# Kernel tuning notes

Hardware: AMD Instinct MI355X
Metric: run time of the kernel (lower is better)

The kernel has to match this reference:

```python
import jax, jax.numpy as jnp
import numpy as np

C = 64
G = 4          # group_number
K = 3          # kernel_size
R = 4          # reduction_ratio -> bottleneck C//R = 16
BN_EPS = 1e-3  # keras BatchNormalization default epsilon


def setup_inputs() -> dict:
    key = jax.random.key(0)
    ks = jax.random.split(key, 8)
    B, H, W = 8, 192, 192
    cr = C // R
    x = jax.random.normal(ks[0], (B, H, W, C), dtype=jnp.float32)
    # kernel_gen: Conv2D 1x1 (C -> C//R), BN, ReLU, Conv2D 1x1 (C//R -> K*K*G)
    w1 = jax.random.normal(ks[1], (C, cr), dtype=jnp.float32) * (1.0 / np.sqrt(C))
    b1 = jnp.zeros((cr,), dtype=jnp.float32)
    gamma = 1.0 + 0.1 * jax.random.normal(ks[2], (cr,), dtype=jnp.float32)
    beta = 0.1 * jax.random.normal(ks[3], (cr,), dtype=jnp.float32)
    mean = 0.1 * jax.random.normal(ks[4], (cr,), dtype=jnp.float32)
    var = jax.random.uniform(ks[5], (cr,), dtype=jnp.float32, minval=0.5, maxval=1.5)
    w2 = jax.random.normal(ks[6], (cr, K * K * G), dtype=jnp.float32) * (1.0 / np.sqrt(cr))
    b2 = jnp.zeros((K * K * G,), dtype=jnp.float32)
    return {"x": x, "w1": w1, "b1": b1, "gamma": gamma, "beta": beta,
            "mean": mean, "var": var, "w2": w2, "b2": b2}


def reference(x, w1, b1, gamma, beta, mean, var, w2, b2):
    B, H, W, Cc = x.shape
    # --- kernel generation (stride=1 -> identity pooling) ---
    t = jnp.einsum('bhwc,cd->bhwd', x, w1) + b1                 # [B,H,W,C//R]
    t = (t - mean) * jax.lax.rsqrt(var + BN_EPS) * gamma + beta  # BN (inference)
    t = jax.nn.relu(t)
    kern = jnp.einsum('bhwd,de->bhwe', t, w2) + b2               # [B,H,W,K*K*G]
    kern = kern.reshape(B, H, W, K * K, 1, G)
    # --- unfold: tf.image.extract_patches SAME, stride 1, patch order (ki,kj,C) ---
    pad = K // 2
    xp = jnp.pad(x, ((0, 0), (pad, pad), (pad, pad), (0, 0)))
    patches = jnp.stack(
        [xp[:, i:i + H, j:j + W, :] for i in range(K) for j in range(K)],
        axis=3)                                                  # [B,H,W,K*K,C]
    unfolded = patches.reshape(B, H, W, K * K, Cc // G, G)
    # --- per-pixel multiply-reduce over patch axis ---
    out = jnp.sum(kern * unfolded, axis=3)                       # [B,H,W,C//G,G]
    return out.reshape(B, H, W, Cc)
```

## Files before the change

kernel.cpp:

```cpp
#include <hip/hip_runtime.h>


#define B_   8
#define H_   192
#define W_   192
#define CR_  16
#define TH_  8
#define TW_  16
#define TILES_X (W_/TW_)
#define TILES_PER_IMG (TILES_X*(H_/TH_))
#define NBLK (B_*TILES_PER_IMG)
#define NPIX (TH_*TW_)

constexpr float BN_EPS = 1e-3f;

template <bool INTERIOR>
__device__ __forceinline__ void col_pass(const float4* __restrict__ x4,
                                         float4* __restrict__ o4,
                                         const float4* __restrict__ s_kern,
                                         int th0, int w, int wl, int c4i)
{
    int co[3];
    int cm = 7;
    #pragma unroll
    for (int tj = 0; tj < 3; ++tj) {
        int ww = w + tj - 1;
        if (!INTERIOR) {
            if ((unsigned)ww >= (unsigned)W_) cm &= ~(1 << tj);
            ww = ww < 0 ? 0 : (ww >= W_ ? W_ - 1 : ww);
        }
        co[tj] = (ww << 4) + c4i;
    }

    float4 ring[5][3];
    int rv = 0;

#define LROW(S, R)                                                          \
    do {                                                                    \
        int rr_ = (R);                                                      \
        if (!INTERIOR) {                                                    \
            if ((unsigned)rr_ < (unsigned)H_) rv |= (1 << (S));             \
            else                              rv &= ~(1 << (S));            \
            rr_ = rr_ < 0 ? 0 : (rr_ >= H_ ? H_ - 1 : rr_);                 \
        }                                                                   \
        const int rb_ = rr_ * (W_ * 16);                                    \
        ring[(S)][0] = x4[rb_ + co[0]];                                     \
        ring[(S)][1] = x4[rb_ + co[1]];                                     \
        ring[(S)][2] = x4[rb_ + co[2]];                                     \
    } while (0)

    LROW(0, th0 - 1);
    LROW(1, th0 + 0);
    LROW(2, th0 + 1);
    LROW(3, th0 + 2);

    #pragma unroll
    for (int i = 0; i < TH_; ++i) {
        if (i < TH_ - 2) { LROW((i + 4) % 5, th0 + i + 3); }

        const float4* kq = &s_kern[(i * TW_ + wl) * 9];
        float4 acc = make_float4(0.f, 0.f, 0.f, 0.f);
        #pragma unroll
        for (int ti = 0; ti < 3; ++ti) {
            const int s = (i + ti) % 5;
            #pragma unroll
            for (int tj = 0; tj < 3; ++tj) {
                float4 kv = kq[ti * 3 + tj];
                if (!INTERIOR) {
                    const bool v = (((rv >> s) & 1) & ((cm >> tj) & 1)) != 0;
                    kv.x = v ? kv.x : 0.f;
                    kv.y = v ? kv.y : 0.f;
                    kv.z = v ? kv.z : 0.f;
                    kv.w = v ? kv.w : 0.f;
                }
                const float4 xv = ring[s][tj];
                acc.x = fmaf(kv.x, xv.x, acc.x);
                acc.y = fmaf(kv.y, xv.y, acc.y);
                acc.z = fmaf(kv.z, xv.z, acc.z);
                acc.w = fmaf(kv.w, xv.w, acc.w);
            }
        }
        o4[(th0 + i) * (W_ * 16) + (w << 4) + c4i] = acc;
    }
#undef LROW
}

__global__ __launch_bounds__(128, 4)
void invol_fused(const float* __restrict__ x,
                 const float* __restrict__ w1,
                 const float* __restrict__ b1,
                 const float* __restrict__ gamma,
                 const float* __restrict__ beta,
                 const float* __restrict__ mean,
                 const float* __restrict__ var,
                 const float* __restrict__ w2,
                 const float* __restrict__ b2,
                 float* __restrict__ out)
{
    __shared__ float4 s_kern[NPIX * 9];

    const int bid = blockIdx.x;
    const int img = bid & 7;
    const int tin = bid >> 3;
    const int th0 = (tin / TILES_X) * TH_;
    const int tw0 = (tin % TILES_X) * TW_;

    const int tid = threadIdx.x;

    {
        const int r = tid >> 4, cc = tid & 15;
        const int h = th0 + r, w = tw0 + cc;
        const float4* xp = reinterpret_cast<const float4*>(
            x + (((size_t)((img * H_ + h) * W_ + w)) << 6));

        float td[CR_];
        #pragma unroll
        for (int d = 0; d < CR_; ++d) td[d] = 0.f;

        #pragma unroll
        for (int c4 = 0; c4 < 16; ++c4) {
            const float4 xv = xp[c4];
            const float xs[4] = {xv.x, xv.y, xv.z, xv.w};
            #pragma unroll
            for (int k = 0; k < 4; ++k) {
                const float* wr = w1 + (c4 * 4 + k) * CR_;
                #pragma unroll
                for (int d = 0; d < CR_; ++d)
                    td[d] = fmaf(xs[k], wr[d], td[d]);
            }
        }

        #pragma unroll
        for (int d = 0; d < CR_; ++d) {
            const float a = gamma[d] * rsqrtf(var[d] + BN_EPS);
            const float c = (b1[d] - mean[d]) * a + beta[d];
            td[d] = fmaxf(fmaf(td[d], a, c), 0.f);
        }

        float ke[36];
        #pragma unroll
        for (int e = 0; e < 36; ++e) ke[e] = b2[e];
        #pragma unroll
        for (int d = 0; d < CR_; ++d) {
            const float t = td[d];
            const float* wr = w2 + d * 36;
            #pragma unroll
            for (int e = 0; e < 36; ++e)
                ke[e] = fmaf(t, wr[e], ke[e]);
        }

        float4* skq = &s_kern[tid * 9];
        #pragma unroll
        for (int t9 = 0; t9 < 9; ++t9)
            skq[t9] = make_float4(ke[t9 * 4 + 0], ke[t9 * 4 + 1],
                                  ke[t9 * 4 + 2], ke[t9 * 4 + 3]);
    }

    __syncthreads();

    const float4* x4 = reinterpret_cast<const float4*>(x) +
                       (size_t)img * (H_ * W_ * 16);
    float4* o4 = reinterpret_cast<float4*>(out) +
                 (size_t)img * (H_ * W_ * 16);

    const bool interior = (th0 > 0) && (th0 + TH_ < H_) &&
                          (tw0 > 0) && (tw0 + TW_ < W_);
    const int wslot = tid >> 4;
    const int c4i   = tid & 15;

    if (interior) {
        col_pass<true >(x4, o4, s_kern, th0, tw0 + wslot,     wslot,     c4i);
        col_pass<true >(x4, o4, s_kern, th0, tw0 + wslot + 8, wslot + 8, c4i);
    } else {
        col_pass<false>(x4, o4, s_kern, th0, tw0 + wslot,     wslot,     c4i);
        col_pass<false>(x4, o4, s_kern, th0, tw0 + wslot + 8, wslot + 8, c4i);
    }
}

extern "C" void kernel_launch(void* const* d_in, const int* in_sizes, int n_in,
                              void* d_out, int out_size, void* d_ws, size_t ws_size,
                              hipStream_t stream) {
    const float* x     = (const float*)d_in[0];
    const float* w1    = (const float*)d_in[1];
    const float* b1    = (const float*)d_in[2];
    const float* gamma = (const float*)d_in[3];
    const float* beta  = (const float*)d_in[4];
    const float* mean  = (const float*)d_in[5];
    const float* var   = (const float*)d_in[6];
    const float* w2    = (const float*)d_in[7];
    const float* b2    = (const float*)d_in[8];
    float* out = (float*)d_out;

    invol_fused<<<dim3(NBLK), dim3(128), 0, stream>>>(
        x, w1, b1, gamma, beta, mean, var, w2, b2, out);
}
```

Before: 199.9 us.

## Interleave both column passes with explicit load/compute software pipelining

Replaces the two sequential per-thread column passes with one pass that handles both columns together, using a 4-slot row ring per column. The next row's loads are issued right after each row's compute, with sched_barrier fences to keep that order. The aim is more memory-level parallelism and overlap of global loads with FMAs in a latency-bound stencil. The register-heavy double ring comes with relaxing launch bounds from 4 to 2 minimum blocks, which can cut occupancy.

```diff
diff --git a/kernel.cpp b/kernel.cpp
--- a/kernel.cpp
+++ b/kernel.cpp
@@ -14,28 +14,22 @@
 
 constexpr float BN_EPS = 1e-3f;
 
-template <bool INTERIOR>
-__device__ __forceinline__ void col_pass(const float4* __restrict__ x4,
-                                         float4* __restrict__ o4,
-                                         const float4* __restrict__ s_kern,
-                                         int th0, int w, int wl, int c4i)
-{
-    int co[3];
-    int cm = 7;
-    #pragma unroll
-    for (int tj = 0; tj < 3; ++tj) {
-        int ww = w + tj - 1;
-        if (!INTERIOR) {
-            if ((unsigned)ww >= (unsigned)W_) cm &= ~(1 << tj);
-            ww = ww < 0 ? 0 : (ww >= W_ ? W_ - 1 : ww);
-        }
-        co[tj] = (ww << 4) + c4i;
-    }
-
-    float4 ring[5][3];
-    int rv = 0;
-
-#define LROW(S, R)                                                          \
+__device__ __forceinline__ float4 mask4(float4 k, bool v) {
+    k.x = v ? k.x : 0.f;
+    k.y = v ? k.y : 0.f;
+    k.z = v ? k.z : 0.f;
+    k.w = v ? k.w : 0.f;
+    return k;
+}
+
+__device__ __forceinline__ void fma4(float4& a, const float4 k, const float4 x) {
+    a.x = fmaf(k.x, x.x, a.x);
+    a.y = fmaf(k.y, x.y, a.y);
+    a.z = fmaf(k.z, x.z, a.z);
+    a.w = fmaf(k.w, x.w, a.w);
+}
+
+#define LROWS(S, R)                                                         \
     do {                                                                    \
         int rr_ = (R);                                                      \
         if (!INTERIOR) {                                                    \
@@ -44,48 +38,97 @@
             rr_ = rr_ < 0 ? 0 : (rr_ >= H_ ? H_ - 1 : rr_);                 \
         }                                                                   \
         const int rb_ = rr_ * (W_ * 16);                                    \
-        ring[(S)][0] = x4[rb_ + co[0]];                                     \
-        ring[(S)][1] = x4[rb_ + co[1]];                                     \
-        ring[(S)][2] = x4[rb_ + co[2]];                                     \
+        rgA[S][0] = x4[rb_ + coA[0]];                                       \
+        rgA[S][1] = x4[rb_ + coA[1]];                                       \
+        rgA[S][2] = x4[rb_ + coA[2]];                                       \
+        rgB[S][0] = x4[rb_ + coB[0]];                                       \
+        rgB[S][1] = x4[rb_ + coB[1]];                                       \
+        rgB[S][2] = x4[rb_ + coB[2]];                                       \
     } while (0)
 
-    LROW(0, th0 - 1);
-    LROW(1, th0 + 0);
-    LROW(2, th0 + 1);
-    LROW(3, th0 + 2);
-
+#define COMP(I)                                                             \
+    do {                                                                    \
+        const float4* kqA_ = &s_kern[((I) * TW_ + wslot) * 9];              \
+        const float4* kqB_ = &s_kern[((I) * TW_ + wslot + 8) * 9];          \
+        float4 aA_ = make_float4(0.f, 0.f, 0.f, 0.f);                       \
+        float4 aB_ = make_float4(0.f, 0.f, 0.f, 0.f);                       \
+        _Pragma("unroll")                                                   \
+        for (int ti_ = 0; ti_ < 3; ++ti_) {                                 \
+            const int s_ = ((I) + ti_) & 3;                                 \
+            _Pragma("unroll")                                               \
+            for (int tj_ = 0; tj_ < 3; ++tj_) {                             \
+                float4 kA_ = kqA_[ti_ * 3 + tj_];                           \
+                float4 kB_ = kqB_[ti_ * 3 + tj_];                           \
+                if (!INTERIOR) {                                            \
+                    kA_ = mask4(kA_, (((rv >> s_) & (cmA >> tj_)) & 1));    \
+                    kB_ = mask4(kB_, (((rv >> s_) & (cmB >> tj_)) & 1));    \
+                }                                                           \
+                fma4(aA_, kA_, rgA[s_][tj_]);                               \
+                fma4(aB_, kB_, rgB[s_][tj_]);                               \
+            }                                                               \
+        }                                                                   \
+        const int ob_ = (th0 + (I)) * (W_ * 16);                            \
+        o4[ob_ + (wA << 4) + c4i] = aA_;                                    \
+        o4[ob_ + (wB << 4) + c4i] = aB_;                                    \
+    } while (0)
+
+#define SFENCE __builtin_amdgcn_sched_barrier(0)
+
+template <bool INTERIOR>
+__device__ __forceinline__ void phase_b(const float4* __restrict__ x4,
+                                        float4* __restrict__ o4,
+                                        const float4* __restrict__ s_kern,
+                                        int th0, int tw0, int tid)
+{
+    const int wslot = tid >> 4;
+    const int c4i   = tid & 15;
+    const int wA = tw0 + wslot;
+    const int wB = tw0 + wslot + 8;
+
+    int coA[3], coB[3];
+    int cmA = 7, cmB = 7;
     #pragma unroll
-    for (int i = 0; i < TH_; ++i) {
-        if (i < TH_ - 2) { LROW((i + 4) % 5, th0 + i + 3); }
-
-        const float4* kq = &s_kern[(i * TW_ + wl) * 9];
-        float4 acc = make_float4(0.f, 0.f, 0.f, 0.f);
-        #pragma unroll
-        for (int ti = 0; ti < 3; ++ti) {
-            const int s = (i + ti) % 5;
-            #pragma unroll
-            for (int tj = 0; tj < 3; ++tj) {
-                float4 kv = kq[ti * 3 + tj];
-                if (!INTERIOR) {
-                    const bool v = (((rv >> s) & 1) & ((cm >> tj) & 1)) != 0;
-                    kv.x = v ? kv.x : 0.f;
-                    kv.y = v ? kv.y : 0.f;
-                    kv.z = v ? kv.z : 0.f;
-                    kv.w = v ? kv.w : 0.f;
-                }
-                const float4 xv = ring[s][tj];
-                acc.x = fmaf(kv.x, xv.x, acc.x);
-                acc.y = fmaf(kv.y, xv.y, acc.y);
-                acc.z = fmaf(kv.z, xv.z, acc.z);
-                acc.w = fmaf(kv.w, xv.w, acc.w);
-            }
-        }
-        o4[(th0 + i) * (W_ * 16) + (w << 4) + c4i] = acc;
+    for (int tj = 0; tj < 3; ++tj) {
+        int wa = wA + tj - 1;
+        int wb = wB + tj - 1;
+        if (!INTERIOR) {
+            if ((unsigned)wa >= (unsigned)W_) cmA &= ~(1 << tj);
+            if ((unsigned)wb >= (unsigned)W_) cmB &= ~(1 << tj);
+            wa = wa < 0 ? 0 : (wa >= W_ ? W_ - 1 : wa);
+            wb = wb < 0 ? 0 : (wb >= W_ ? W_ - 1 : wb);
+        }
+        coA[tj] = (wa << 4) + c4i;
+        coB[tj] = (wb << 4) + c4i;
     }
-#undef LROW
-}
-
-__global__ __launch_bounds__(128, 4)
+
+    float4 rgA[4][3], rgB[4][3];
+    int rv = 0xF;
+
+    LROWS(0, th0 - 1);
+    LROWS(1, th0 + 0);
+    LROWS(2, th0 + 1);
+    LROWS(3, th0 + 2);
+    SFENCE;
+    COMP(0); LROWS(0, th0 + 3);
+    SFENCE;
+    COMP(1); LROWS(1, th0 + 4);
+    SFENCE;
+    COMP(2); LROWS(2, th0 + 5);
+    SFENCE;
+    COMP(3); LROWS(3, th0 + 6);
+    SFENCE;
+    COMP(4); LROWS(0, th0 + 7);
+    SFENCE;
+    COMP(5); LROWS(1, th0 + 8);
+    SFENCE;
+    COMP(6);
+    COMP(7);
+}
+
+#undef LROWS
+#undef COMP
+
+__global__ __launch_bounds__(128, 2)
 void invol_fused(const float* __restrict__ x,
                  const float* __restrict__ w1,
                  const float* __restrict__ b1,
@@ -165,16 +208,10 @@
 
     const bool interior = (th0 > 0) && (th0 + TH_ < H_) &&
                           (tw0 > 0) && (tw0 + TW_ < W_);
-    const int wslot = tid >> 4;
-    const int c4i   = tid & 15;
-
-    if (interior) {
-        col_pass<true >(x4, o4, s_kern, th0, tw0 + wslot,     wslot,     c4i);
-        col_pass<true >(x4, o4, s_kern, th0, tw0 + wslot + 8, wslot + 8, c4i);
-    } else {
-        col_pass<false>(x4, o4, s_kern, th0, tw0 + wslot,     wslot,     c4i);
-        col_pass<false>(x4, o4, s_kern, th0, tw0 + wslot + 8, wslot + 8, c4i);
-    }
+    if (interior)
+        phase_b<true >(x4, o4, s_kern, th0, tw0, tid);
+    else
+        phase_b<false>(x4, o4, s_kern, th0, tw0, tid);
 }
 
 extern "C" void kernel_launch(void* const* d_in, const int* in_sizes, int n_in,
```

Result: faster. 174.7 us (-12.6%).
